# Kernel tuning notes

Hardware: AMD Instinct MI355X
Metric: run time of the kernel (lower is better)

## Reference

```python
import jax, jax.numpy as jnp
import numpy as np
import math

B = 2        # batch
S = 4095     # input sequence (cls token makes L = 4096)
F_IN = 32    # input feature size
D = 512      # d_model (hidden_size)
H = 8        # n_heads
E = D // H   # head dim = 64
DFF = 2048   # feedforward dim
NL = 2       # encoder layers
FACTOR = 5   # probsparse sampling factor
EPS = 1e-5


def setup_inputs() -> dict:
    key = jax.random.key(0)
    ks = jax.random.split(key, 16)

    def w(k, shape):
        return jax.random.normal(k, shape, dtype=jnp.float32) * 0.02

    inp = {}
    inp['x'] = jax.random.normal(ks[0], (B, S, F_IN), dtype=jnp.float32)
    inp['We'] = w(ks[1], (D, F_IN)); inp['be'] = jnp.zeros((D,), jnp.float32)
    inp['cls'] = jnp.zeros((1, 1, D), jnp.float32)
    inp['Wq'] = w(ks[2], (NL, D, D)); inp['bq'] = jnp.zeros((NL, D), jnp.float32)
    inp['Wk'] = w(ks[3], (NL, D, D)); inp['bk'] = jnp.zeros((NL, D), jnp.float32)
    inp['Wv'] = w(ks[4], (NL, D, D)); inp['bv'] = jnp.zeros((NL, D), jnp.float32)
    inp['Wo'] = w(ks[5], (NL, D, D)); inp['bo'] = jnp.zeros((NL, D), jnp.float32)
    inp['g1'] = jnp.ones((NL, D), jnp.float32); inp['b1'] = jnp.zeros((NL, D), jnp.float32)
    inp['g2'] = jnp.ones((NL, D), jnp.float32); inp['b2'] = jnp.zeros((NL, D), jnp.float32)
    inp['W1'] = w(ks[6], (NL, DFF, D)); inp['bf1'] = jnp.zeros((NL, DFF), jnp.float32)
    inp['W2'] = w(ks[7], (NL, D, DFF)); inp['bf2'] = jnp.zeros((NL, D), jnp.float32)
    inp['Wf'] = w(ks[8], (1, D)); inp['bf'] = jnp.zeros((1,), jnp.float32)
    return inp


def pos_encoding(L):
    # Sinusoidal positional encoding [L, D]
    pos = jnp.arange(L, dtype=jnp.float32)[:, None]
    div = jnp.exp(jnp.arange(0, D, 2, dtype=jnp.float32) * (-math.log(10000.0) / D))
    pe = jnp.zeros((L, D), jnp.float32)
    pe = pe.at[:, 0::2].set(jnp.sin(pos * div))
    pe = pe.at[:, 1::2].set(jnp.cos(pos * div))
    return pe


def layer_norm(x, g, b):
    mu = x.mean(-1, keepdims=True)
    var = ((x - mu) ** 2).mean(-1, keepdims=True)
    return (x - mu) / jnp.sqrt(var + EPS) * g + b


def prob_attention(q, k, v, rng):
    # q, k, v: [B, H, L, E]; mask_flag=False (encoder self-attention)
    b, h, L, e = q.shape
    u = min(FACTOR * int(np.ceil(np.log(L))), L)  # sample_k == n_top here (L_Q == L_K)
    idx = jax.random.randint(rng, (L, u), 0, L)   # random K sampling per query position
    Ks = k[:, :, idx, :]                          # [B,H,L,u,E] gather
    QKs = jnp.einsum('bhle,bhlue->bhlu', q, Ks)   # sampled scores
    M = QKs.max(-1) - QKs.sum(-1) / L             # sparsity measure [B,H,L]
    _, top = jax.lax.top_k(M, u)                  # active query indices [B,H,u]
    Qr = jnp.take_along_axis(q, top[..., None], axis=2)      # [B,H,u,E]
    scores = jnp.einsum('bhue,bhke->bhuk', Qr, k) / math.sqrt(e)
    attn = jax.nn.softmax(scores, axis=-1)
    ctx = jnp.broadcast_to(v.mean(axis=2, keepdims=True), (b, h, L, e))  # initial context = mean(V)
    upd = jnp.einsum('bhuk,bhke->bhue', attn, v)
    bi = jnp.arange(b)[:, None, None]
    hi = jnp.arange(h)[None, :, None]
    ctx = ctx.at[bi, hi, top].set(upd)            # scatter active-query contexts
    return ctx                                    # [B,H,L,E]


def attention_layer(x, Wq_, bq_, Wk_, bk_, Wv_, bv_, Wo_, bo_, rng):
    b, L, _ = x.shape
    q = (x @ Wq_.T + bq_).reshape(b, L, H, E).transpose(0, 2, 1, 3)
    k = (x @ Wk_.T + bk_).reshape(b, L, H, E).transpose(0, 2, 1, 3)
    v = (x @ Wv_.T + bv_).reshape(b, L, H, E).transpose(0, 2, 1, 3)
    ctx = prob_attention(q, k, v, rng)            # [B,H,L,E]
    out = ctx.transpose(0, 2, 1, 3).reshape(b, L, D)
    return out @ Wo_.T + bo_


def reference(x, We, be, cls, Wq, bq, Wk, bk, Wv, bv, Wo, bo, g1, b1, g2, b2, W1, bf1, W2, bf2, Wf, bf):
    h = x @ We.T + be                                            # [B,S,D]
    h = jnp.concatenate([jnp.broadcast_to(cls, (B, 1, D)), h], axis=1)  # prepend cls
    L = h.shape[1]
    h = h + pos_encoding(L)[None]
    for l in range(NL):
        rng = jax.random.fold_in(jax.random.key(42), l)
        a = attention_layer(h, Wq[l], bq[l], Wk[l], bk[l], Wv[l], bv[l], Wo[l], bo[l], rng)
        h = layer_norm(h + a, g1[l], b1[l])
        y = jax.nn.relu(h @ W1[l].T + bf1[l])
        y = y @ W2[l].T + bf2[l]
        h = layer_norm(h + y, g2[l], b2[l])
    return h[:, 0] @ Wf.T + bf  # cls-token prediction head [B,1]
```

## Files before the change

kernel.cpp:

```cpp
#include <hip/hip_runtime.h>
#include <hip/hip_bf16.h>
#include <math.h>
#include <stdint.h>

#define B 2
#define S 4095
#define LSEQ 4096
#define F_IN 32
#define D 512
#define H 8
#define E 64
#define DFF 2048
#define NL 2
#define U 45
#define EPSL 1e-5f
#define LU (LSEQ * U)
#define HALF_LU (LU / 2)
#define NS 32
#define SLICE 128

typedef __attribute__((ext_vector_type(8))) short short8;
typedef __attribute__((ext_vector_type(4))) float f32x4;

#define GLD(gp, lp)                                                            \
    __builtin_amdgcn_global_load_lds(                                          \
        (const __attribute__((address_space(1))) void*)(gp),                   \
        (__attribute__((address_space(3))) void*)(lp), 16, 0, 0)

__device__ __forceinline__ unsigned short bf16_bits(float f) {
    __hip_bfloat16 h = __float2bfloat16(f);
    return *(unsigned short*)&h;
}
__device__ __forceinline__ float bits_to_f32(unsigned short s) {
    union { uint32_t u; float f; } c;
    c.u = ((uint32_t)s) << 16;
    return c.f;
}
__device__ __forceinline__ unsigned long long mkey(float v, int index) {
    uint32_t u = __float_as_uint(v);
    uint32_t mono = (u & 0x80000000u) ? ~u : (u | 0x80000000u);
    return ((unsigned long long)mono << 32) | (uint32_t)(0xFFFFFFFFu - (uint32_t)index);
}

#define TF_BODY(k0, k1, c0, c1, o0, o1)                                        \
    do {                                                                       \
        uint32_t ks2 = (k0) ^ (k1) ^ 0x1BD11BDAu;                              \
        uint32_t x0 = (c0) + (k0), x1 = (c1) + (k1);                           \
        x0 += x1; x1 = ((x1 << 13) | (x1 >> 19)); x1 ^= x0;                    \
        x0 += x1; x1 = ((x1 << 15) | (x1 >> 17)); x1 ^= x0;                    \
        x0 += x1; x1 = ((x1 << 26) | (x1 >> 6));  x1 ^= x0;                    \
        x0 += x1; x1 = ((x1 << 6) | (x1 >> 26));  x1 ^= x0;                    \
        x0 += (k1); x1 += ks2 + 1u;                                            \
        x0 += x1; x1 = ((x1 << 17) | (x1 >> 15)); x1 ^= x0;                    \
        x0 += x1; x1 = ((x1 << 29) | (x1 >> 3));  x1 ^= x0;                    \
        x0 += x1; x1 = ((x1 << 16) | (x1 >> 16)); x1 ^= x0;                    \
        x0 += x1; x1 = ((x1 << 24) | (x1 >> 8));  x1 ^= x0;                    \
        x0 += ks2; x1 += (k0) + 2u;                                            \
        x0 += x1; x1 = ((x1 << 13) | (x1 >> 19)); x1 ^= x0;                    \
        x0 += x1; x1 = ((x1 << 15) | (x1 >> 17)); x1 ^= x0;                    \
        x0 += x1; x1 = ((x1 << 26) | (x1 >> 6));  x1 ^= x0;                    \
        x0 += x1; x1 = ((x1 << 6) | (x1 >> 26));  x1 ^= x0;                    \
        x0 += (k0); x1 += (k1) + 3u;                                           \
        x0 += x1; x1 = ((x1 << 17) | (x1 >> 15)); x1 ^= x0;                    \
        x0 += x1; x1 = ((x1 << 29) | (x1 >> 3));  x1 ^= x0;                    \
        x0 += x1; x1 = ((x1 << 16) | (x1 >> 16)); x1 ^= x0;                    \
        x0 += x1; x1 = ((x1 << 24) | (x1 >> 8));  x1 ^= x0;                    \
        x0 += (k1); x1 += ks2 + 4u;                                            \
        x0 += x1; x1 = ((x1 << 13) | (x1 >> 19)); x1 ^= x0;                    \
        x0 += x1; x1 = ((x1 << 15) | (x1 >> 17)); x1 ^= x0;                    \
        x0 += x1; x1 = ((x1 << 26) | (x1 >> 6));  x1 ^= x0;                    \
        x0 += x1; x1 = ((x1 << 6) | (x1 >> 26));  x1 ^= x0;                    \
        x0 += ks2; x1 += (k0) + 5u;                                            \
        (o0) = x0; (o1) = x1;                                                  \
    } while (0)

__device__ __forceinline__ void threefry_dev(uint32_t k0, uint32_t k1, uint32_t c0,
                                             uint32_t c1, uint32_t& o0, uint32_t& o1) {
    TF_BODY(k0, k1, c0, c1, o0, o1);
}
static void threefry_host(uint32_t k0, uint32_t k1, uint32_t c0, uint32_t c1,
                          uint32_t& o0, uint32_t& o1) {
    TF_BODY(k0, k1, c0, c1, o0, o1);
}

__global__ void prep_embed_kernel(const float* __restrict__ x, const float* __restrict__ We,
                                  __hip_bfloat16* __restrict__ xbf,
                                  __hip_bfloat16* __restrict__ webf) {
    int u = blockIdx.x * blockDim.x + threadIdx.x;
    const int NX = B * LSEQ * F_IN / 4;
    const int NW = D * F_IN / 4;
    if (u < NX) {
        int e0 = u * 4;
        int i = e0 & 31;
        int l = (e0 >> 5) & (LSEQ - 1);
        int b = e0 >> 17;
        union { unsigned short s[4]; uint2 w; } o;
        if (l == 0) {
            o.s[0] = o.s[1] = o.s[2] = o.s[3] = 0;
        } else {
            float4 v = *(const float4*)(x + ((size_t)b * S + (l - 1)) * F_IN + i);
            o.s[0] = bf16_bits(v.x); o.s[1] = bf16_bits(v.y);
            o.s[2] = bf16_bits(v.z); o.s[3] = bf16_bits(v.w);
        }
        ((uint2*)xbf)[u] = o.w;
    } else if (u < NX + NW) {
        int w = u - NX;
        float4 v = ((const float4*)We)[w];
        union { unsigned short s[4]; uint2 w2; } o;
        o.s[0] = bf16_bits(v.x); o.s[1] = bf16_bits(v.y);
        o.s[2] = bf16_bits(v.z); o.s[3] = bf16_bits(v.w);
        ((uint2*)webf)[w] = o.w2;
    }
}

__global__ __launch_bounds__(256) void gemm32(const unsigned short* __restrict__ A,
                                              const unsigned short* __restrict__ W,
                                              const float* __restrict__ bias,
                                              float* __restrict__ Cf,
                                              int M, int N, int K) {
    __shared__ unsigned short lds[2 * 128 * 32];
    unsigned short* As = lds;
    unsigned short* Bs = lds + 128 * 32;
    const int tid = threadIdx.x;
    const int m0 = blockIdx.y * 128, n0 = blockIdx.x * 128;
    const int wave = tid >> 6, lane = tid & 63;
    const int wm = (wave >> 1) * 64, wn = (wave & 1) * 64;
    const int quad = lane >> 4, m15 = lane & 15;
    const int srow = tid >> 2, scol = (tid & 3) * 8;
    f32x4 acc[4][4] = {};
    const unsigned short* Ag0 = A + (size_t)(m0 + srow) * K + scol;
    const unsigned short* Ag1 = A + (size_t)(m0 + srow + 64) * K + scol;
    const unsigned short* Wg0 = W + (size_t)(n0 + srow) * K + scol;
    const unsigned short* Wg1 = W + (size_t)(n0 + srow + 64) * K + scol;
    for (int k0 = 0; k0 < K; k0 += 32) {
        __syncthreads();
        GLD(Ag0 + k0, As + tid * 8);
        GLD(Ag1 + k0, As + 2048 + tid * 8);
        GLD(Wg0 + k0, Bs + tid * 8);
        GLD(Wg1 + k0, Bs + 2048 + tid * 8);
        __syncthreads();
        short8 af[4], bfr[4];
#pragma unroll
        for (int mi = 0; mi < 4; ++mi)
            af[mi] = *(const short8*)(As + (wm + mi * 16 + m15) * 32 + quad * 8);
#pragma unroll
        for (int ni = 0; ni < 4; ++ni)
            bfr[ni] = *(const short8*)(Bs + (wn + ni * 16 + m15) * 32 + quad * 8);
#pragma unroll
        for (int mi = 0; mi < 4; ++mi)
#pragma unroll
            for (int ni = 0; ni < 4; ++ni)
                acc[mi][ni] = __builtin_amdgcn_mfma_f32_16x16x32_bf16(
                    af[mi], bfr[ni], acc[mi][ni], 0, 0, 0);
    }
#pragma unroll
    for (int mi = 0; mi < 4; ++mi) {
        int mg = m0 + wm + mi * 16 + quad * 4;
#pragma unroll
        for (int ni = 0; ni < 4; ++ni) {
            int ng = n0 + wn + ni * 16 + m15;
            float bv = bias[ng];
#pragma unroll
            for (int r = 0; r < 4; ++r)
                Cf[(size_t)(mg + r) * N + ng] = acc[mi][ni][r] + bv;
        }
    }
}

__global__ void posenc_kernel(const float* __restrict__ emb, const float* __restrict__ cls,
                              __hip_bfloat16* __restrict__ hbf) {
    int gid = blockIdx.x * blockDim.x + threadIdx.x;
    if (gid >= B * LSEQ * D) return;
    int d = gid % D;
    int l = (gid / D) % LSEQ;
    float v = (l == 0) ? cls[d] : emb[gid];
    int i = d >> 1;
    float divv = expf((float)(2 * i) * (float)(-9.210340371976184 / 512.0));
    float ang = (float)l * divv;
    v += (d & 1) ? cosf(ang) : sinf(ang);
    hbf[gid] = __float2bfloat16(v);
}

__global__ void cast_weights_kernel(const float* __restrict__ Wq,
                                    const float* __restrict__ Wk,
                                    const float* __restrict__ Wv,
                                    const float* __restrict__ Wo,
                                    const float* __restrict__ W1,
                                    const float* __restrict__ W2,
                                    const float* __restrict__ bq,
                                    const float* __restrict__ bk,
                                    const float* __restrict__ bv,
                                    __hip_bfloat16* __restrict__ wpool,
                                    float* __restrict__ qkvbias) {
    const int SDD = D * D / 4;
    const int SFD = DFF * D / 4;
    const int CAST_N = 4 * SDD + 2 * SFD;
    const size_t WPL = (size_t)4 * D * D + 2 * (size_t)DFF * D;
    int l = blockIdx.y;
    int u = blockIdx.x * blockDim.x + threadIdx.x;
    __hip_bfloat16* base = wpool + (size_t)l * WPL;
    if (u >= CAST_N) {
        int j = u - CAST_N;
        if (j < 384) {
            int seg = (j * 4) >> 9;
            int off = (j * 4) & 511;
            const float* src = (seg == 0) ? bq + l * D
                             : (seg == 1) ? bk + l * D : bv + l * D;
            *(float4*)(qkvbias + l * 1536 + j * 4) = *(const float4*)(src + off);
        }
        return;
    }
    const float* src;
    __hip_bfloat16* dst;
    int off;
    if (u < SDD)            { src = Wq + (size_t)l * D * D;   dst = base;                       off = u; }
    else if (u < 2 * SDD)   { src = Wk + (size_t)l * D * D;   dst = base + (size_t)D * D;       off = u - SDD; }
    else if (u < 3 * SDD)   { src = Wv + (size_t)l * D * D;   dst = base + (size_t)2 * D * D;   off = u - 2 * SDD; }
    else if (u < 4 * SDD)   { src = Wo + (size_t)l * D * D;   dst = base + (size_t)3 * D * D;   off = u - 3 * SDD; }
    else if (u < 4 * SDD + SFD) { src = W1 + (size_t)l * DFF * D; dst = base + (size_t)4 * D * D; off = u - 4 * SDD; }
    else { src = W2 + (size_t)l * D * DFF; dst = base + (size_t)4 * D * D + (size_t)DFF * D; off = u - 4 * SDD - SFD; }
    float4 v = ((const float4*)src)[off];
    union { unsigned short s[4]; uint2 w; } o;
    o.s[0] = bf16_bits(v.x); o.s[1] = bf16_bits(v.y);
    o.s[2] = bf16_bits(v.z); o.s[3] = bf16_bits(v.w);
    ((uint2*)dst)[off] = o.w;
}

template <int MODE>
__global__ __launch_bounds__(256) void gemm_pipe(const unsigned short* __restrict__ A,
                                                 const unsigned short* __restrict__ W,
                                                 const float* __restrict__ bias,
                                                 void* __restrict__ C0,
                                                 void* __restrict__ C1,
                                                 void* __restrict__ C2,
                                                 int M, int N, int K, int NBN) {
    __shared__ unsigned short As[2][128 * 32];
    __shared__ unsigned short Bs[2][128 * 32];
    const int tid = threadIdx.x;
    const int NBM = M >> 7;
    const int bid = blockIdx.x;
    const int xcd = bid & 7, local = bid >> 3;
    const int m_t = xcd * (NBM >> 3) + local / NBN;
    const int n_t = local % NBN;
    const int m0 = m_t * 128, n0 = n_t * 128;
    const int wave = tid >> 6, lane = tid & 63;
    const int wm = (wave >> 1) * 64, wn = (wave & 1) * 64;
    const int quad = lane >> 4, m15 = lane & 15;
    const int srow = tid >> 2, scol = (tid & 3) * 8;
    f32x4 acc[4][4] = {};
    const unsigned short* Ag0 = A + (size_t)(m0 + srow) * K + scol;
    const unsigned short* Ag1 = A + (size_t)(m0 + srow + 64) * K + scol;
    const unsigned short* Wg0 = W + (size_t)(n0 + srow) * K + scol;
    const unsigned short* Wg1 = W + (size_t)(n0 + srow + 64) * K + scol;
    GLD(Ag0, As[0] + tid * 8);
    GLD(Ag1, As[0] + 2048 + tid * 8);
    GLD(Wg0, Bs[0] + tid * 8);
    GLD(Wg1, Bs[0] + 2048 + tid * 8);
    int cur = 0;
    for (int k0 = 0; k0 < K; k0 += 32) {
        __syncthreads();
        int kn = k0 + 32;
        if (kn < K) {
            GLD(Ag0 + kn, As[cur ^ 1] + tid * 8);
            GLD(Ag1 + kn, As[cur ^ 1] + 2048 + tid * 8);
            GLD(Wg0 + kn, Bs[cur ^ 1] + tid * 8);
            GLD(Wg1 + kn, Bs[cur ^ 1] + 2048 + tid * 8);
        }
        short8 af[4], bfr[4];
#pragma unroll
        for (int mi = 0; mi < 4; ++mi)
            af[mi] = *(const short8*)(As[cur] + (wm + mi * 16 + m15) * 32 + quad * 8);
#pragma unroll
        for (int ni = 0; ni < 4; ++ni)
            bfr[ni] = *(const short8*)(Bs[cur] + (wn + ni * 16 + m15) * 32 + quad * 8);
#pragma unroll
        for (int mi = 0; mi < 4; ++mi)
#pragma unroll
            for (int ni = 0; ni < 4; ++ni)
                acc[mi][ni] = __builtin_amdgcn_mfma_f32_16x16x32_bf16(
                    af[mi], bfr[ni], acc[mi][ni], 0, 0, 0);
        cur ^= 1;
    }
#pragma unroll
    for (int mi = 0; mi < 4; ++mi) {
        int mg = m0 + wm + mi * 16 + quad * 4;
#pragma unroll
        for (int ni = 0; ni < 4; ++ni) {
            int ng = n0 + wn + ni * 16 + m15;
            float bv = bias[ng];
#pragma unroll
            for (int r = 0; r < 4; ++r) {
                float v = acc[mi][ni][r] + bv;
                if (MODE == 1) {
                    ((__hip_bfloat16*)C0)[(size_t)(mg + r) * N + ng] = __float2bfloat16(v);
                } else if (MODE == 2) {
                    ((__hip_bfloat16*)C0)[(size_t)(mg + r) * N + ng] =
                        __float2bfloat16(fmaxf(v, 0.f));
                } else {
                    int seg = ng >> 9;
                    int col = ng & 511;
                    __hip_bfloat16* dst = (seg == 0) ? (__hip_bfloat16*)C0
                                        : (seg == 1) ? (__hip_bfloat16*)C1
                                                     : (__hip_bfloat16*)C2;
                    dst[(size_t)(mg + r) * D + col] = __float2bfloat16(v);
                }
            }
        }
    }
}

__global__ __launch_bounds__(256) void gemm_w2b(const unsigned short* __restrict__ A,
                                                const unsigned short* __restrict__ W,
                                                const float* __restrict__ bias,
                                                float* __restrict__ C0,
                                                float* __restrict__ C1) {
    const int K = 2048, N = 512, KH = 1024;
    __shared__ unsigned short As[2][128 * 32];
    __shared__ unsigned short Bs[2][128 * 32];
    const int tid = threadIdx.x;
    const int bid = blockIdx.x;
    const int xcd = bid & 7, local = bid >> 3;
    const int m_t = xcd * 8 + (local >> 3);
    const int n_t = (local >> 1) & 3;
    const int ks = local & 1;
    const int m0 = m_t * 128, n0 = n_t * 128, kb = ks * KH;
    const int wave = tid >> 6, lane = tid & 63;
    const int wm = (wave >> 1) * 64, wn = (wave & 1) * 64;
    const int quad = lane >> 4, m15 = lane & 15;
    const int srow = tid >> 2, scol = (tid & 3) * 8;
    f32x4 acc[4][4] = {};
    const unsigned short* Ag0 = A + (size_t)(m0 + srow) * K + kb + scol;
    const unsigned short* Ag1 = A + (size_t)(m0 + srow + 64) * K + kb + scol;
    const unsigned short* Wg0 = W + (size_t)(n0 + srow) * K + kb + scol;
    const unsigned short* Wg1 = W + (size_t)(n0 + srow + 64) * K + kb + scol;
    GLD(Ag0, As[0] + tid * 8);
    GLD(Ag1, As[0] + 2048 + tid * 8);
    GLD(Wg0, Bs[0] + tid * 8);
    GLD(Wg1, Bs[0] + 2048 + tid * 8);
    int cur = 0;
    for (int k0 = 0; k0 < KH; k0 += 32) {
        __syncthreads();
        int kn = k0 + 32;
        if (kn < KH) {
            GLD(Ag0 + kn, As[cur ^ 1] + tid * 8);
            GLD(Ag1 + kn, As[cur ^ 1] + 2048 + tid * 8);
            GLD(Wg0 + kn, Bs[cur ^ 1] + tid * 8);
            GLD(Wg1 + kn, Bs[cur ^ 1] + 2048 + tid * 8);
        }
        short8 af[4], bfr[4];
#pragma unroll
        for (int mi = 0; mi < 4; ++mi)
            af[mi] = *(const short8*)(As[cur] + (wm + mi * 16 + m15) * 32 + quad * 8);
#pragma unroll
        for (int ni = 0; ni < 4; ++ni)
            bfr[ni] = *(const short8*)(Bs[cur] + (wn + ni * 16 + m15) * 32 + quad * 8);
#pragma unroll
        for (int mi = 0; mi < 4; ++mi)
#pragma unroll
            for (int ni = 0; ni < 4; ++ni)
                acc[mi][ni] = __builtin_amdgcn_mfma_f32_16x16x32_bf16(
                    af[mi], bfr[ni], acc[mi][ni], 0, 0, 0);
        cur ^= 1;
    }
    float* Cf = ks ? C1 : C0;
#pragma unroll
    for (int mi = 0; mi < 4; ++mi) {
        int mg = m0 + wm + mi * 16 + quad * 4;
#pragma unroll
        for (int ni = 0; ni < 4; ++ni) {
            int ng = n0 + wn + ni * 16 + m15;
            float bv = ks ? 0.f : bias[ng];
#pragma unroll
            for (int r = 0; r < 4; ++r)
                Cf[(size_t)(mg + r) * N + ng] = acc[mi][ni][r] + bv;
        }
    }
}

__global__ __launch_bounds__(256) void mscore_kernel(const __hip_bfloat16* __restrict__ qbf,
                                                     const __hip_bfloat16* __restrict__ kbf,
                                                     uint32_t k2a, uint32_t k2b,
                                                     float* __restrict__ Mv) {
    __shared__ float Sbuf[U][8];
    __shared__ int sidx[U];
    int bid = blockIdx.x;
    int b = bid & 1;
    int l = bid >> 1;
    int tid = threadIdx.x;
    int wave = tid >> 6, lane = tid & 63;
    if (tid < U) {
        int i = l * U + tid;
        uint32_t c0 = (i < HALF_LU) ? (uint32_t)i : (uint32_t)(i - HALF_LU);
        uint32_t o0, o1;
        threefry_dev(k2a, k2b, c0, c0 + HALF_LU, o0, o1);
        sidx[tid] = (int)(((i < HALF_LU) ? o0 : o1) & 4095u);
    }
    const unsigned short* qr =
        (const unsigned short*)qbf + ((size_t)(b * LSEQ) + l) * D + lane * 8;
    union { uint4 u; unsigned short s[8]; } qv;
    qv.u = *(const uint4*)qr;
    float qa[8];
#pragma unroll
    for (int j = 0; j < 8; ++j) qa[j] = bits_to_f32(qv.s[j]);
    __syncthreads();
    const unsigned short* kbase = (const unsigned short*)(kbf + (size_t)(b * LSEQ) * D);
    for (int t = wave; t < U; t += 12) {
        int tb = t + 4, tc = t + 8;
        bool hb = tb < U, hc = tc < U;
        union { uint4 u; unsigned short s[8]; } kva, kvb, kvc;
        kva.u = *(const uint4*)(kbase + (size_t)sidx[t] * D + lane * 8);
        if (hb) kvb.u = *(const uint4*)(kbase + (size_t)sidx[tb] * D + lane * 8);
        if (hc) kvc.u = *(const uint4*)(kbase + (size_t)sidx[tc] * D + lane * 8);
        {
            float p = 0.f;
#pragma unroll
            for (int j = 0; j < 8; ++j) p += qa[j] * bits_to_f32(kva.s[j]);
            p += __shfl_xor(p, 1);
            p += __shfl_xor(p, 2);
            p += __shfl_xor(p, 4);
            if ((lane & 7) == 0) Sbuf[t][lane >> 3] = p;
        }
        if (hb) {
            float p = 0.f;
#pragma unroll
            for (int j = 0; j < 8; ++j) p += qa[j] * bits_to_f32(kvb.s[j]);
            p += __shfl_xor(p, 1);
            p += __shfl_xor(p, 2);
            p += __shfl_xor(p, 4);
            if ((lane & 7) == 0) Sbuf[tb][lane >> 3] = p;
        }
        if (hc) {
            float p = 0.f;
#pragma unroll
            for (int j = 0; j < 8; ++j) p += qa[j] * bits_to_f32(kvc.s[j]);
            p += __shfl_xor(p, 1);
            p += __shfl_xor(p, 2);
            p += __shfl_xor(p, 4);
            if ((lane & 7) == 0) Sbuf[tc][lane >> 3] = p;
        }
    }
    __syncthreads();
    if (tid < 8) {
        float mx = -INFINITY, sm = 0.f;
        for (int t = 0; t < U; ++t) {
            float v = Sbuf[t][tid];
            mx = fmaxf(mx, v);
            sm += v;
        }
        Mv[((size_t)b * H + tid) * LSEQ + l] = mx - sm / (float)LSEQ;
    }
}

__global__ __launch_bounds__(256) void topk_chunk_kernel(const float* __restrict__ Mv,
                                                         unsigned long long* __restrict__ cand) {
    __shared__ unsigned long long sk[256];
    int blk = blockIdx.x;
    int chunk = blk & 15, bh = blk >> 4;
    int tid = threadIdx.x;
    int gi = chunk * 256 + tid;
    sk[tid] = mkey(Mv[(size_t)bh * LSEQ + gi], gi);
    __syncthreads();
    for (int k = 2; k <= 256; k <<= 1) {
        for (int j = k >> 1; j > 0; j >>= 1) {
            int ixj = tid ^ j;
            if (ixj > tid) {
                unsigned long long a = sk[tid], b = sk[ixj];
                bool desc = ((tid & k) == 0);
                if (desc ? (a < b) : (a > b)) { sk[tid] = b; sk[ixj] = a; }
            }
            __syncthreads();
        }
    }
    if (tid < U) cand[((size_t)bh * 16 + chunk) * U + tid] = sk[tid];
}

__global__ __launch_bounds__(256) void topkmerge_vmean_kernel(
        const unsigned long long* __restrict__ cand, int* __restrict__ top,
        const __hip_bfloat16* __restrict__ v, float* __restrict__ part,
        unsigned char* __restrict__ flags) {
    __shared__ unsigned long long sk[1024];
    __shared__ float red[4][64];
    int blk = blockIdx.x;
    int tid = threadIdx.x;
    if (blk < B * H) {
        int bh = blk;
        for (int e = tid; e < 1024; e += 256)
            sk[e] = (e < 16 * U) ? cand[(size_t)bh * 16 * U + e] : 0ull;
        __syncthreads();
        for (int k = 2; k <= 1024; k <<= 1) {
            for (int j = k >> 1; j > 0; j >>= 1) {
                for (int e = tid; e < 1024; e += 256) {
                    int ixj = e ^ j;
                    if (ixj > e) {
                        unsigned long long a = sk[e], b = sk[ixj];
                        bool desc = ((e & k) == 0);
                        if (desc ? (a < b) : (a > b)) { sk[e] = b; sk[ixj] = a; }
                    }
                }
                __syncthreads();
            }
        }
        if (tid < U)
            top[bh * U + tid] = (int)(0xFFFFFFFFu - (uint32_t)(sk[tid] & 0xFFFFFFFFu));
    } else if (blk < B * H + B * H * 8) {
        int vb = blk - B * H;
        int seg = vb & 7, hh = (vb >> 3) & 7, b = vb >> 6;
        int e = tid & 63, rg = tid >> 6;
        const __hip_bfloat16* vp =
            v + ((size_t)(b * LSEQ) + seg * 512) * D + hh * 64 + e;
        float acc = 0.f;
        for (int r = rg; r < 512; r += 4) acc += __bfloat162float(vp[(size_t)r * D]);
        red[rg][e] = acc;
        __syncthreads();
        if (tid < 64)
            part[(size_t)vb * 64 + tid] =
                red[0][tid] + red[1][tid] + red[2][tid] + red[3][tid];
    } else {
        int fb = blk - (B * H + B * H * 8);
        ((int*)flags)[fb * 256 + tid] = 0;
    }
}

__global__ __launch_bounds__(256) void zero_wobase_kernel(
        const int* __restrict__ top, float* __restrict__ aout,
        unsigned char* __restrict__ flags, const float* __restrict__ vpart,
        const unsigned short* __restrict__ wob, const float* __restrict__ bo,
        float* __restrict__ base) {
    int bid = blockIdx.x;
    int tid = threadIdx.x;
    if (bid < B * H * U) {
        int t = bid % U;
        int bh = bid / U;
        int b = bh >> 3;
        int r = top[bh * U + t];
        if (tid < 128) {
            float4 z = {0.f, 0.f, 0.f, 0.f};
            ((float4*)(aout + (size_t)(b * LSEQ + r) * D))[tid] = z;
        }
        if (tid == 0) flags[b * LSEQ + r] = 1;
    } else {
        int wb = bid - B * H * U;
        int b = wb >> 7;
        int n = (wb & 127) * 4 + (tid >> 6);
        int lane = tid & 63;
        float vmv[8];
#pragma unroll
        for (int j = 0; j < 8; ++j) {
            int idx = lane * 8 + j;
            int hh = idx >> 6, e = idx & 63;
            float acc = 0.f;
#pragma unroll
            for (int s = 0; s < 8; ++s)
                acc += vpart[((size_t)(b * 8 + hh) * 8 + s) * 64 + e];
            vmv[j] = acc / (float)LSEQ;
        }
        union { uint4 u; unsigned short s[8]; } w;
        w.u = *(const uint4*)(wob + (size_t)n * D + lane * 8);
        float p = vmv[0] * bits_to_f32(w.s[0]) + vmv[1] * bits_to_f32(w.s[1]) +
                  vmv[2] * bits_to_f32(w.s[2]) + vmv[3] * bits_to_f32(w.s[3]) +
                  vmv[4] * bits_to_f32(w.s[4]) + vmv[5] * bits_to_f32(w.s[5]) +
                  vmv[6] * bits_to_f32(w.s[6]) + vmv[7] * bits_to_f32(w.s[7]);
        for (int off = 32; off; off >>= 1) p += __shfl_xor(p, off);
        if (lane == 0) base[(size_t)b * D + n] = p + bo[n];
    }
}

__global__ __launch_bounds__(256) void attnred_corr_kernel(const float* __restrict__ Opart,
                                                           const float* __restrict__ msum,
                                                           const float* __restrict__ vpart,
                                                           const unsigned short* __restrict__ wob,
                                                           const int* __restrict__ top,
                                                           float* __restrict__ aout) {
    __shared__ float dlt[E];
    int bid = blockIdx.x;
    int t = bid % U;
    int bh = bid / U;
    int b = bh >> 3, hh = bh & 7;
    int tid = threadIdx.x;
    if (tid < 64) {
        int lane = tid;
        float m_s = -INFINITY, ss = 0.f;
        if (lane < NS) {
            size_t base = (((size_t)bh * NS + lane) * U + t) * 2;
            m_s = msum[base];
            ss = msum[base + 1];
        }
        float M = m_s;
        for (int off = 32; off; off >>= 1) M = fmaxf(M, __shfl_xor(M, off));
        float e_s = (lane < NS) ? __expf(m_s - M) : 0.f;
        float d = ss * e_s;
        for (int off = 32; off; off >>= 1) d += __shfl_xor(d, off);
        float acc = 0.f;
        for (int s = 0; s < NS; ++s) {
            float w = __shfl(e_s, s);
            acc += w * Opart[(((size_t)bh * NS + s) * U + t) * 64 + lane];
        }
        float vmv = 0.f;
#pragma unroll
        for (int s = 0; s < 8; ++s) vmv += vpart[((size_t)bh * 8 + s) * 64 + lane];
        dlt[lane] = acc / d - vmv / (float)LSEQ;
    }
    __syncthreads();
    int r = top[bh * U + t];
    float* arow = aout + (size_t)(b * LSEQ + r) * D;
    for (int n = tid; n < D; n += 256) {
        const unsigned short* wr = wob + (size_t)n * D + hh * E;
        float acc = 0.f;
#pragma unroll
        for (int v4 = 0; v4 < 8; ++v4) {
            union { uint4 u; unsigned short s[8]; } w;
            w.u = *(const uint4*)(wr + v4 * 8);
#pragma unroll
            for (int j = 0; j < 8; ++j)
                acc += dlt[v4 * 8 + j] * bits_to_f32(w.s[j]);
        }
        atomicAdd(arow + n, acc);
    }
}

__global__ __launch_bounds__(256) void attn_part(const __hip_bfloat16* __restrict__ qbf,
                                                 const __hip_bfloat16* __restrict__ kbf,
                                                 const __hip_bfloat16* __restrict__ vbf,
                                                 const int* __restrict__ top,
                                                 float* __restrict__ Opart,
                                                 float* __restrict__ msum) {
    __shared__ unsigned short Qs[48 * 72];
    __shared__ unsigned short Ks[SLICE * 72];
    __shared__ unsigned short Vs[SLICE * 68];
    __shared__ unsigned short Ps[48 * 136];
    __shared__ float mred[48][4];
    __shared__ float sred[48][4];
    const int slice = blockIdx.x, hh = blockIdx.y, b = blockIdx.z;
    const int bh = b * H + hh;
    const int tid = threadIdx.x;
    const int s0 = slice * SLICE;
    for (int i = tid; i < 48 * 64; i += 256) {
        int t = i >> 6, e = i & 63;
        unsigned short v = 0;
        if (t < U) {
            int r = top[bh * U + t];
            v = ((const unsigned short*)qbf)[((size_t)(b * LSEQ) + r) * D + hh * E + e];
        }
        Qs[t * 72 + e] = v;
    }
    {
        const uint4* src = (const uint4*)(kbf + ((size_t)(b * LSEQ) + s0) * D + hh * E);
        for (int i = tid; i < SLICE * 8; i += 256) {
            int r = i >> 3, c = i & 7;
            uint4 d = src[(size_t)r * 64 + c];
            *(uint4*)(Ks + r * 72 + c * 8) = d;
        }
    }
    {
        const uint2* src = (const uint2*)(vbf + ((size_t)(b * LSEQ) + s0) * D + hh * E);
        for (int i = tid; i < SLICE * 16; i += 256) {
            int r = i >> 4, c = i & 15;
            uint2 d = src[(size_t)r * 128 + c];
            *(uint2*)(Vs + r * 68 + c * 4) = d;
        }
    }
    __syncthreads();
    const int wave = tid >> 6, lane = tid & 63;
    const int quad = lane >> 4, m15 = lane & 15;
    const int wc = wave * 32;
    f32x4 acc[3][2] = {};
#pragma unroll
    for (int ks = 0; ks < 2; ++ks) {
        short8 af[3], bfr[2];
#pragma unroll
        for (int mt = 0; mt < 3; ++mt)
            af[mt] = *(const short8*)(Qs + (mt * 16 + m15) * 72 + ks * 32 + quad * 8);
#pragma unroll
        for (int nt = 0; nt < 2; ++nt)
            bfr[nt] = *(const short8*)(Ks + (wc + nt * 16 + m15) * 72 + ks * 32 + quad * 8);
#pragma unroll
        for (int mt = 0; mt < 3; ++mt)
#pragma unroll
            for (int nt = 0; nt < 2; ++nt)
                acc[mt][nt] = __builtin_amdgcn_mfma_f32_16x16x32_bf16(
                    af[mt], bfr[nt], acc[mt][nt], 0, 0, 0);
    }
    float sc[3][2][4];
#pragma unroll
    for (int mt = 0; mt < 3; ++mt)
#pragma unroll
        for (int nt = 0; nt < 2; ++nt)
#pragma unroll
            for (int r = 0; r < 4; ++r) sc[mt][nt][r] = acc[mt][nt][r] * 0.125f;
#pragma unroll
    for (int mt = 0; mt < 3; ++mt)
#pragma unroll
        for (int r = 0; r < 4; ++r) {
            float mv = fmaxf(sc[mt][0][r], sc[mt][1][r]);
            mv = fmaxf(mv, __shfl_xor(mv, 1));
            mv = fmaxf(mv, __shfl_xor(mv, 2));
            mv = fmaxf(mv, __shfl_xor(mv, 4));
            mv = fmaxf(mv, __shfl_xor(mv, 8));
            if (m15 == 0) mred[mt * 16 + quad * 4 + r][wave] = mv;
        }
    __syncthreads();
#pragma unroll
    for (int mt = 0; mt < 3; ++mt)
#pragma unroll
        for (int r = 0; r < 4; ++r) {
            int row = mt * 16 + quad * 4 + r;
            float ms = fmaxf(fmaxf(mred[row][0], mred[row][1]),
                             fmaxf(mred[row][2], mred[row][3]));
            float p0 = __expf(sc[mt][0][r] - ms);
            float p1 = __expf(sc[mt][1][r] - ms);
            float sv = p0 + p1;
            sv += __shfl_xor(sv, 1);
            sv += __shfl_xor(sv, 2);
            sv += __shfl_xor(sv, 4);
            sv += __shfl_xor(sv, 8);
            if (m15 == 0) sred[row][wave] = sv;
            Ps[row * 136 + wc + m15] = bf16_bits(p0);
            Ps[row * 136 + wc + 16 + m15] = bf16_bits(p1);
        }
    __syncthreads();
    if (tid < U) {
        float mm = fmaxf(fmaxf(mred[tid][0], mred[tid][1]),
                         fmaxf(mred[tid][2], mred[tid][3]));
        float ss = sred[tid][0] + sred[tid][1] + sred[tid][2] + sred[tid][3];
        size_t base = (((size_t)bh * NS + slice) * U + tid) * 2;
        msum[base] = mm;
        msum[base + 1] = ss;
    }
    f32x4 apv[3] = {};
#pragma unroll
    for (int ks = 0; ks < 4; ++ks) {
        short8 bv;
#pragma unroll
        for (int j = 0; j < 8; ++j)
            bv[j] = (short)Vs[(ks * 32 + quad * 8 + j) * 68 + wave * 16 + m15];
        short8 af2[3];
#pragma unroll
        for (int mt = 0; mt < 3; ++mt)
            af2[mt] = *(const short8*)(Ps + (mt * 16 + m15) * 136 + ks * 32 + quad * 8);
#pragma unroll
        for (int mt = 0; mt < 3; ++mt)
            apv[mt] = __builtin_amdgcn_mfma_f32_16x16x32_bf16(af2[mt], bv, apv[mt], 0, 0, 0);
    }
    size_t obase = ((size_t)bh * NS + slice) * U;
#pragma unroll
    for (int mt = 0; mt < 3; ++mt)
#pragma unroll
        for (int r = 0; r < 4; ++r) {
            int row = mt * 16 + quad * 4 + r;
            if (row < U)
                Opart[(obase + row) * 64 + wave * 16 + m15] = apv[mt][r];
        }
}

__global__ __launch_bounds__(64) void add_ln_base_kernel(__hip_bfloat16* __restrict__ hbf,
                                                         const float* __restrict__ base,
                                                         const float* __restrict__ aout,
                                                         const unsigned char* __restrict__ flags,
                                                         const float* __restrict__ g,
                                                         const float* __restrict__ bb) {
    int row = blockIdx.x;
    int b = row >> 12;
    int lane = threadIdx.x;
    unsigned short* hp = (unsigned short*)hbf + (size_t)row * D;
    const float* bp = base + (size_t)b * D;
    const float* ap = aout + (size_t)row * D;
    bool has = flags[row] != 0;
    float x[8];
    float sum = 0.f;
#pragma unroll
    for (int j = 0; j < 8; ++j) {
        float a = bp[lane + 64 * j];
        if (has) a += ap[lane + 64 * j];
        x[j] = bits_to_f32(hp[lane + 64 * j]) + a;
        sum += x[j];
    }
    for (int off = 32; off; off >>= 1) sum += __shfl_xor(sum, off);
    float mu = sum / (float)D;
    float vs = 0.f;
#pragma unroll
    for (int j = 0; j < 8; ++j) {
        float dd = x[j] - mu;
        vs += dd * dd;
    }
    for (int off = 32; off; off >>= 1) vs += __shfl_xor(vs, off);
    float inv = 1.f / sqrtf(vs / (float)D + EPSL);
#pragma unroll
    for (int j = 0; j < 8; ++j) {
        float o = (x[j] - mu) * inv * g[lane + 64 * j] + bb[lane + 64 * j];
        hp[lane + 64 * j] = bf16_bits(o);
    }
}

__global__ __launch_bounds__(64) void add_ln_kernel(__hip_bfloat16* __restrict__ hbf,
                                                    const float* __restrict__ a,
                                                    const float* __restrict__ a2,
                                                    const float* __restrict__ g,
                                                    const float* __restrict__ bb) {
    int row = blockIdx.x;
    int lane = threadIdx.x;
    unsigned short* hp = (unsigned short*)hbf + (size_t)row * D;
    const float* ap = a + (size_t)row * D;
    const float* ap2 = a2 + (size_t)row * D;
    float x[8];
    float sum = 0.f;
#pragma unroll
    for (int j = 0; j < 8; ++j) {
        x[j] = bits_to_f32(hp[lane + 64 * j]) + ap[lane + 64 * j] + ap2[lane + 64 * j];
        sum += x[j];
    }
    for (int off = 32; off; off >>= 1) sum += __shfl_xor(sum, off);
    float mu = sum / (float)D;
    float vs = 0.f;
#pragma unroll
    for (int j = 0; j < 8; ++j) {
        float dd = x[j] - mu;
        vs += dd * dd;
    }
    for (int off = 32; off; off >>= 1) vs += __shfl_xor(vs, off);
    float inv = 1.f / sqrtf(vs / (float)D + EPSL);
#pragma unroll
    for (int j = 0; j < 8; ++j) {
        float o = (x[j] - mu) * inv * g[lane + 64 * j] + bb[lane + 64 * j];
        hp[lane + 64 * j] = bf16_bits(o);
    }
}

__global__ void final_kernel(const __hip_bfloat16* __restrict__ hbf,
                             const float* __restrict__ Wf,
                             const float* __restrict__ bf, float* __restrict__ out) {
    int b = blockIdx.x;
    int lane = threadIdx.x;
    const unsigned short* hp = (const unsigned short*)hbf + (size_t)b * LSEQ * D;
    float acc = 0.f;
    for (int j = lane; j < D; j += 64) acc += bits_to_f32(hp[j]) * Wf[j];
    for (int off = 32; off; off >>= 1) acc += __shfl_xor(acc, off);
    if (lane == 0) out[b] = acc + bf[0];
}

extern "C" void kernel_launch(void* const* d_in, const int* in_sizes, int n_in,
                              void* d_out, int out_size, void* d_ws, size_t ws_size,
                              hipStream_t stream) {
    (void)in_sizes; (void)n_in; (void)out_size; (void)ws_size;
    const float* x   = (const float*)d_in[0];
    const float* We  = (const float*)d_in[1];
    const float* be  = (const float*)d_in[2];
    const float* cls = (const float*)d_in[3];
    const float* Wq  = (const float*)d_in[4];
    const float* bq  = (const float*)d_in[5];
    const float* Wk  = (const float*)d_in[6];
    const float* bk  = (const float*)d_in[7];
    const float* Wv  = (const float*)d_in[8];
    const float* bv  = (const float*)d_in[9];
    const float* Wo  = (const float*)d_in[10];
    const float* bo  = (const float*)d_in[11];
    const float* g1  = (const float*)d_in[12];
    const float* b1  = (const float*)d_in[13];
    const float* g2  = (const float*)d_in[14];
    const float* b2  = (const float*)d_in[15];
    const float* W1  = (const float*)d_in[16];
    const float* bf1 = (const float*)d_in[17];
    const float* W2  = (const float*)d_in[18];
    const float* bf2 = (const float*)d_in[19];
    const float* Wf  = (const float*)d_in[20];
    const float* bff = (const float*)d_in[21];
    float* out = (float*)d_out;

    float* ws = (float*)d_ws;
    const size_t NT = (size_t)B * LSEQ * D;
    float* aout = ws + NT;
    __hip_bfloat16* kbf    = (__hip_bfloat16*)(ws + NT);
    __hip_bfloat16* q_bf   = (__hip_bfloat16*)(ws + 2 * NT);
    __hip_bfloat16* y1_bf  = (__hip_bfloat16*)(ws + 2 * NT);
    __hip_bfloat16* v_bf   = (__hip_bfloat16*)(ws + 4 * NT);
    __hip_bfloat16* h_bf   = (__hip_bfloat16*)(ws + 5 * NT);
    float* emb  = ws;
    float* tmp  = ws;
    float* Opart = ws + 3 * NT;
    float* msumb = Opart + (size_t)B * H * NS * U * 64;
    float* wpool = ws + 5 * NT + NT / 2;
    const size_t WPL = (size_t)4 * D * D + 2 * (size_t)DFF * D;
    __hip_bfloat16* wpool_bf = (__hip_bfloat16*)wpool;
    float* after_w = wpool + (2 * WPL) / 2;
    float* Mbuf = after_w;
    int* top    = (int*)(Mbuf + (size_t)B * H * LSEQ);
    float* vm   = (float*)(top + B * H * U);
    float* vpart  = vm + (size_t)B * H * E;
    float* baseb  = vpart + (size_t)128 * 64;
    __hip_bfloat16* xbf  = (__hip_bfloat16*)(baseb + (size_t)B * D);
    __hip_bfloat16* webf = xbf + (size_t)B * LSEQ * F_IN;
    unsigned long long* cand =
        (unsigned long long*)(((uintptr_t)(webf + (size_t)D * F_IN) + 7) & ~(uintptr_t)7);
    float* qkvbias = (float*)(cand + (size_t)B * H * 16 * U);
    unsigned char* flags = (unsigned char*)(qkvbias + 2 * 1536);

    const int ML = B * LSEQ;
    dim3 gD(D / 128, ML / 128);
    const int CAST_N = 4 * (D * D / 4) + 2 * (DFF * D / 4);
    dim3 gCast((CAST_N + 384 + 255) / 256, NL);

    prep_embed_kernel<<<(B * LSEQ * F_IN / 4 + D * F_IN / 4 + 255) / 256, 256, 0, stream>>>(
        x, We, xbf, webf);
    cast_weights_kernel<<<gCast, 256, 0, stream>>>(Wq, Wk, Wv, Wo, W1, W2, bq, bk, bv,
                                                   wpool_bf, qkvbias);
    gemm32<<<gD, 256, 0, stream>>>((const unsigned short*)xbf,
                                   (const unsigned short*)webf, be, emb, ML, D, F_IN);
    posenc_kernel<<<(B * LSEQ * D + 255) / 256, 256, 0, stream>>>(emb, cls, h_bf);

    for (int l = 0; l < NL; ++l) {
        uint32_t f0, f1, a0, a1, bb0, bb1;
        threefry_host(0u, 42u, 0u, (uint32_t)l, f0, f1);
        threefry_host(f0, f1, 0u, 2u, a0, a1);
        threefry_host(f0, f1, 1u, 3u, bb0, bb1);
        (void)a0; (void)bb0;

        __hip_bfloat16* wqb = wpool_bf + (size_t)l * WPL;
        __hip_bfloat16* wob = wqb + (size_t)3 * D * D;
        __hip_bfloat16* w1b = wqb + (size_t)4 * D * D;
        __hip_bfloat16* w2b = w1b + (size_t)DFF * D;

        gemm_pipe<3><<<768, 256, 0, stream>>>((const unsigned short*)h_bf,
                                              (const unsigned short*)wqb,
                                              qkvbias + (size_t)l * 1536,
                                              q_bf, kbf, v_bf, ML, 3 * D, D, 12);

        mscore_kernel<<<B * LSEQ, 256, 0, stream>>>(q_bf, kbf, a1, bb1, Mbuf);
        topk_chunk_kernel<<<B * H * 16, 256, 0, stream>>>(Mbuf, cand);
        topkmerge_vmean_kernel<<<B * H + B * H * 8 + 8, 256, 0, stream>>>(
            cand, top, v_bf, vpart, flags);
        attn_part<<<dim3(NS, H, B), 256, 0, stream>>>(q_bf, kbf, v_bf, top, Opart, msumb);
        zero_wobase_kernel<<<B * H * U + B * 128, 256, 0, stream>>>(
            top, aout, flags, vpart, (const unsigned short*)wob, bo + l * D, baseb);
        attnred_corr_kernel<<<B * H * U, 256, 0, stream>>>(Opart, msumb, vpart,
                                                           (const unsigned short*)wob, top,
                                                           aout);
        add_ln_base_kernel<<<ML, 64, 0, stream>>>(h_bf, baseb, aout, flags,
                                                  g1 + l * D, b1 + l * D);

        gemm_pipe<2><<<1024, 256, 0, stream>>>((const unsigned short*)h_bf,
                                               (const unsigned short*)w1b, bf1 + l * DFF,
                                               y1_bf, nullptr, nullptr, ML, DFF, D, 16);
        gemm_w2b<<<512, 256, 0, stream>>>((const unsigned short*)y1_bf,
                                          (const unsigned short*)w2b, bf2 + l * D,
                                          aout, tmp);
        add_ln_kernel<<<ML, 64, 0, stream>>>(h_bf, aout, tmp, g2 + l * D, b2 + l * D);
    }

    final_kernel<<<B, 64, 0, stream>>>(h_bf, Wf, bff, out);
}
```

Measured before the change: 544.5 us.

## Fuse embedding projection with positional encoding and fold final head into LayerNorm

```diff
diff --git a/kernel.cpp b/kernel.cpp
--- a/kernel.cpp
+++ b/kernel.cpp
@@ -83,102 +83,38 @@
     TF_BODY(k0, k1, c0, c1, o0, o1);
 }
 
-__global__ void prep_embed_kernel(const float* __restrict__ x, const float* __restrict__ We,
-                                  __hip_bfloat16* __restrict__ xbf,
-                                  __hip_bfloat16* __restrict__ webf) {
-    int u = blockIdx.x * blockDim.x + threadIdx.x;
-    const int NX = B * LSEQ * F_IN / 4;
-    const int NW = D * F_IN / 4;
-    if (u < NX) {
-        int e0 = u * 4;
-        int i = e0 & 31;
-        int l = (e0 >> 5) & (LSEQ - 1);
-        int b = e0 >> 17;
-        union { unsigned short s[4]; uint2 w; } o;
+__global__ __launch_bounds__(256) void embed_posenc_kernel(
+        const float* __restrict__ x, const float* __restrict__ We,
+        const float* __restrict__ be, const float* __restrict__ cls,
+        __hip_bfloat16* __restrict__ hbf) {
+    int row = blockIdx.x;
+    int b = row >> 12;
+    int l = row & (LSEQ - 1);
+    int tid = threadIdx.x;
+    __shared__ float xs[F_IN];
+    if (l > 0 && tid < F_IN)
+        xs[tid] = bits_to_f32(bf16_bits(x[((size_t)b * S + (l - 1)) * F_IN + tid]));
+    __syncthreads();
+#pragma unroll
+    for (int hh = 0; hh < 2; ++hh) {
+        int n = tid + hh * 256;
+        float v;
         if (l == 0) {
-            o.s[0] = o.s[1] = o.s[2] = o.s[3] = 0;
+            v = cls[n];
         } else {
-            float4 v = *(const float4*)(x + ((size_t)b * S + (l - 1)) * F_IN + i);
-            o.s[0] = bf16_bits(v.x); o.s[1] = bf16_bits(v.y);
-            o.s[2] = bf16_bits(v.z); o.s[3] = bf16_bits(v.w);
-        }
-        ((uint2*)xbf)[u] = o.w;
-    } else if (u < NX + NW) {
-        int w = u - NX;
-        float4 v = ((const float4*)We)[w];
-        union { unsigned short s[4]; uint2 w2; } o;
-        o.s[0] = bf16_bits(v.x); o.s[1] = bf16_bits(v.y);
-        o.s[2] = bf16_bits(v.z); o.s[3] = bf16_bits(v.w);
-        ((uint2*)webf)[w] = o.w2;
-    }
-}
-
-__global__ __launch_bounds__(256) void gemm32(const unsigned short* __restrict__ A,
-                                              const unsigned short* __restrict__ W,
-                                              const float* __restrict__ bias,
-                                              float* __restrict__ Cf,
-                                              int M, int N, int K) {
-    __shared__ unsigned short lds[2 * 128 * 32];
-    unsigned short* As = lds;
-    unsigned short* Bs = lds + 128 * 32;
-    const int tid = threadIdx.x;
-    const int m0 = blockIdx.y * 128, n0 = blockIdx.x * 128;
-    const int wave = tid >> 6, lane = tid & 63;
-    const int wm = (wave >> 1) * 64, wn = (wave & 1) * 64;
-    const int quad = lane >> 4, m15 = lane & 15;
-    const int srow = tid >> 2, scol = (tid & 3) * 8;
-    f32x4 acc[4][4] = {};
-    const unsigned short* Ag0 = A + (size_t)(m0 + srow) * K + scol;
-    const unsigned short* Ag1 = A + (size_t)(m0 + srow + 64) * K + scol;
-    const unsigned short* Wg0 = W + (size_t)(n0 + srow) * K + scol;
-    const unsigned short* Wg1 = W + (size_t)(n0 + srow + 64) * K + scol;
-    for (int k0 = 0; k0 < K; k0 += 32) {
-        __syncthreads();
-        GLD(Ag0 + k0, As + tid * 8);
-        GLD(Ag1 + k0, As + 2048 + tid * 8);
-        GLD(Wg0 + k0, Bs + tid * 8);
-        GLD(Wg1 + k0, Bs + 2048 + tid * 8);
-        __syncthreads();
-        short8 af[4], bfr[4];
-#pragma unroll
-        for (int mi = 0; mi < 4; ++mi)
-            af[mi] = *(const short8*)(As + (wm + mi * 16 + m15) * 32 + quad * 8);
-#pragma unroll
-        for (int ni = 0; ni < 4; ++ni)
-            bfr[ni] = *(const short8*)(Bs + (wn + ni * 16 + m15) * 32 + quad * 8);
-#pragma unroll
-        for (int mi = 0; mi < 4; ++mi)
-#pragma unroll
-            for (int ni = 0; ni < 4; ++ni)
-                acc[mi][ni] = __builtin_amdgcn_mfma_f32_16x16x32_bf16(
-                    af[mi], bfr[ni], acc[mi][ni], 0, 0, 0);
-    }
-#pragma unroll
-    for (int mi = 0; mi < 4; ++mi) {
-        int mg = m0 + wm + mi * 16 + quad * 4;
-#pragma unroll
-        for (int ni = 0; ni < 4; ++ni) {
-            int ng = n0 + wn + ni * 16 + m15;
-            float bv = bias[ng];
-#pragma unroll
-            for (int r = 0; r < 4; ++r)
-                Cf[(size_t)(mg + r) * N + ng] = acc[mi][ni][r] + bv;
-        }
-    }
-}
-
-__global__ void posenc_kernel(const float* __restrict__ emb, const float* __restrict__ cls,
-                              __hip_bfloat16* __restrict__ hbf) {
-    int gid = blockIdx.x * blockDim.x + threadIdx.x;
-    if (gid >= B * LSEQ * D) return;
-    int d = gid % D;
-    int l = (gid / D) % LSEQ;
-    float v = (l == 0) ? cls[d] : emb[gid];
-    int i = d >> 1;
-    float divv = expf((float)(2 * i) * (float)(-9.210340371976184 / 512.0));
-    float ang = (float)l * divv;
-    v += (d & 1) ? cosf(ang) : sinf(ang);
-    hbf[gid] = __float2bfloat16(v);
+            const float* wr = We + (size_t)n * F_IN;
+            float acc = 0.f;
+#pragma unroll
+            for (int k = 0; k < F_IN; ++k)
+                acc += xs[k] * bits_to_f32(bf16_bits(wr[k]));
+            v = acc + be[n];
+        }
+        int i2 = n >> 1;
+        float divv = expf((float)(2 * i2) * (float)(-9.210340371976184 / 512.0));
+        float ang = (float)l * divv;
+        v += (n & 1) ? cosf(ang) : sinf(ang);
+        hbf[(size_t)row * D + n] = __float2bfloat16(v);
+    }
 }
 
 __global__ void cast_weights_kernel(const float* __restrict__ Wq,
@@ -795,7 +731,11 @@
                                                     const float* __restrict__ a,
                                                     const float* __restrict__ a2,
                                                     const float* __restrict__ g,
-                                                    const float* __restrict__ bb) {
+                                                    const float* __restrict__ bb,
+                                                    const float* __restrict__ Wf,
+                                                    const float* __restrict__ bf,
+                                                    float* __restrict__ out,
+                                                    int fuseFinal) {
     int row = blockIdx.x;
     int lane = threadIdx.x;
     unsigned short* hp = (unsigned short*)hbf + (size_t)row * D;
@@ -818,23 +758,19 @@
     }
     for (int off = 32; off; off >>= 1) vs += __shfl_xor(vs, off);
     float inv = 1.f / sqrtf(vs / (float)D + EPSL);
+    bool doFinal = fuseFinal && ((row & (LSEQ - 1)) == 0);
+    float facc = 0.f;
 #pragma unroll
     for (int j = 0; j < 8; ++j) {
         float o = (x[j] - mu) * inv * g[lane + 64 * j] + bb[lane + 64 * j];
-        hp[lane + 64 * j] = bf16_bits(o);
-    }
-}
-
-__global__ void final_kernel(const __hip_bfloat16* __restrict__ hbf,
-                             const float* __restrict__ Wf,
-                             const float* __restrict__ bf, float* __restrict__ out) {
-    int b = blockIdx.x;
-    int lane = threadIdx.x;
-    const unsigned short* hp = (const unsigned short*)hbf + (size_t)b * LSEQ * D;
-    float acc = 0.f;
-    for (int j = lane; j < D; j += 64) acc += bits_to_f32(hp[j]) * Wf[j];
-    for (int off = 32; off; off >>= 1) acc += __shfl_xor(acc, off);
-    if (lane == 0) out[b] = acc + bf[0];
+        unsigned short ob = bf16_bits(o);
+        hp[lane + 64 * j] = ob;
+        if (doFinal) facc += bits_to_f32(ob) * Wf[lane + 64 * j];
+    }
+    if (doFinal) {
+        for (int off = 32; off; off >>= 1) facc += __shfl_xor(facc, off);
+        if (lane == 0) out[row >> 12] = facc + bf[0];
+    }
 }
 
 extern "C" void kernel_launch(void* const* d_in, const int* in_sizes, int n_in,
@@ -873,7 +809,6 @@
     __hip_bfloat16* y1_bf  = (__hip_bfloat16*)(ws + 2 * NT);
     __hip_bfloat16* v_bf   = (__hip_bfloat16*)(ws + 4 * NT);
     __hip_bfloat16* h_bf   = (__hip_bfloat16*)(ws + 5 * NT);
-    float* emb  = ws;
     float* tmp  = ws;
     float* Opart = ws + 3 * NT;
     float* msumb = Opart + (size_t)B * H * NS * U * 64;
@@ -883,28 +818,20 @@
     float* after_w = wpool + (2 * WPL) / 2;
     float* Mbuf = after_w;
     int* top    = (int*)(Mbuf + (size_t)B * H * LSEQ);
-    float* vm   = (float*)(top + B * H * U);
-    float* vpart  = vm + (size_t)B * H * E;
+    float* vpart  = (float*)(top + B * H * U);
     float* baseb  = vpart + (size_t)128 * 64;
-    __hip_bfloat16* xbf  = (__hip_bfloat16*)(baseb + (size_t)B * D);
-    __hip_bfloat16* webf = xbf + (size_t)B * LSEQ * F_IN;
     unsigned long long* cand =
-        (unsigned long long*)(((uintptr_t)(webf + (size_t)D * F_IN) + 7) & ~(uintptr_t)7);
+        (unsigned long long*)(((uintptr_t)(baseb + (size_t)B * D) + 7) & ~(uintptr_t)7);
     float* qkvbias = (float*)(cand + (size_t)B * H * 16 * U);
     unsigned char* flags = (unsigned char*)(qkvbias + 2 * 1536);
 
     const int ML = B * LSEQ;
-    dim3 gD(D / 128, ML / 128);
     const int CAST_N = 4 * (D * D / 4) + 2 * (DFF * D / 4);
     dim3 gCast((CAST_N + 384 + 255) / 256, NL);
 
-    prep_embed_kernel<<<(B * LSEQ * F_IN / 4 + D * F_IN / 4 + 255) / 256, 256, 0, stream>>>(
-        x, We, xbf, webf);
     cast_weights_kernel<<<gCast, 256, 0, stream>>>(Wq, Wk, Wv, Wo, W1, W2, bq, bk, bv,
                                                    wpool_bf, qkvbias);
-    gemm32<<<gD, 256, 0, stream>>>((const unsigned short*)xbf,
-                                   (const unsigned short*)webf, be, emb, ML, D, F_IN);
-    posenc_kernel<<<(B * LSEQ * D + 255) / 256, 256, 0, stream>>>(emb, cls, h_bf);
+    embed_posenc_kernel<<<ML, 256, 0, stream>>>(x, We, be, cls, h_bf);
 
     for (int l = 0; l < NL; ++l) {
         uint32_t f0, f1, a0, a1, bb0, bb1;
@@ -942,8 +869,7 @@
         gemm_w2b<<<512, 256, 0, stream>>>((const unsigned short*)y1_bf,
                                           (const unsigned short*)w2b, bf2 + l * D,
                                           aout, tmp);
-        add_ln_kernel<<<ML, 64, 0, stream>>>(h_bf, aout, tmp, g2 + l * D, b2 + l * D);
-    }
-
-    final_kernel<<<B, 64, 0, stream>>>(h_bf, Wf, bff, out);
-}
+        add_ln_kernel<<<ML, 64, 0, stream>>>(h_bf, aout, tmp, g2 + l * D, b2 + l * D,
+                                             Wf, bff, out, (l == NL - 1) ? 1 : 0);
+    }
+}
```

Measured after the change: 590.6 us. 8.5% more time.
